# Optimization experiments

Measured on AMD Instinct MI355X. Metric: run time of the kernel, lower is better.

## Reference

```python
import jax, jax.numpy as jnp
import numpy as np

H = 3.0        # args.h smoothing length
N_NODES = 100000
DIM_HIDDEN = 128
D = 3


def setup_inputs() -> dict:
    key = jax.random.key(0)
    ks = jax.random.split(key, 10)
    E = 1600000
    v = jax.random.normal(ks[0], (N_NODES, D), dtype=jnp.float32)
    r_ij = jax.random.normal(ks[1], (E, D), dtype=jnp.float32)
    edge_index = jax.random.randint(ks[2], (2, E), 0, N_NODES, dtype=jnp.int64)
    # teacher MLP params: [1+D] -> dim_hidden -> dim_hidden -> 1
    def lin(k, fan_in, fan_out):
        bound = 1.0 / np.sqrt(fan_in)
        kw, kb = jax.random.split(k)
        W = jax.random.uniform(kw, (fan_out, fan_in), jnp.float32, -bound, bound)
        b = jax.random.uniform(kb, (fan_out,), jnp.float32, -bound, bound)
        return W, b
    W0, b0 = lin(ks[3], 1 + D, DIM_HIDDEN)
    W1, b1 = lin(ks[4], DIM_HIDDEN, DIM_HIDDEN)
    W2, b2 = lin(ks[5], DIM_HIDDEN, 1)
    return {"v": v, "r_ij": r_ij, "W0": W0, "b0": b0, "W1": W1, "b1": b1,
            "W2": W2, "b2": b2, "edge_index": edge_index}


def _teacher(x, W0, b0, W1, b1, W2, b2):
    x = jax.nn.silu(x @ W0.T + b0)
    x = jax.nn.silu(x @ W1.T + b1)
    return x @ W2.T + b2  # [E, 1]


def _scatter_mean(x, idx, n):
    s = jax.ops.segment_sum(x, idx, num_segments=n)
    c = jax.ops.segment_sum(jnp.ones((idx.shape[0], 1), x.dtype), idx, num_segments=n)
    return s / jnp.maximum(c, 1.0)


def reference(v, r_ij, W0, b0, W1, b1, W2, b2, edge_index):
    i = edge_index[0]
    j = edge_index[1]
    v_ij = v[i] - v[j]                                   # [E, D] gather-diff
    r_ = jnp.sqrt(jnp.sum(r_ij * r_ij, axis=-1, keepdims=True)) / H  # [E, 1]
    m_i = _teacher(jnp.concatenate([r_, v_ij], axis=-1), W0, b0, W1, b1, W2, b2)
    m_j = _teacher(jnp.concatenate([r_, -v_ij], axis=-1), W0, b0, W1, b1, W2, b2)
    S = _scatter_mean(m_i, i, N_NODES) + _scatter_mean(m_j, j, N_NODES)  # [N, 1]
    return S
```

## Files before the change

### kernel.cpp

```cpp
#include <hip/hip_runtime.h>

typedef unsigned short ushort_t;
typedef __bf16 bf16x8 __attribute__((ext_vector_type(8)));
typedef __bf16 bf16x2 __attribute__((ext_vector_type(2)));
typedef float f32x4 __attribute__((ext_vector_type(4)));

__device__ __forceinline__ ushort_t f2bf(float f) {
    unsigned u;
    __builtin_memcpy(&u, &f, 4);
    u += 0x7fffu + ((u >> 16) & 1u);
    return (ushort_t)(u >> 16);
}

__device__ __forceinline__ float silu(float x) {
    float e = __builtin_amdgcn_exp2f(x * -1.442695040888963f);
    return x * __builtin_amdgcn_rcpf(1.0f + e);
}

__device__ __forceinline__ float rdlane(float v, int l) {
    return __builtin_bit_cast(float, __builtin_amdgcn_readlane(__builtin_bit_cast(int, v), l));
}


#define CNT_UNIT 65536.0

__global__ __launch_bounds__(256, 2) void mlp_kernel(
    const float* __restrict__ v,
    const float* __restrict__ rij,
    const float* __restrict__ W0,
    const float* __restrict__ b0,
    const float* __restrict__ W1,
    const float* __restrict__ b1,
    const float* __restrict__ W2,
    const float* __restrict__ b2,
    const int* __restrict__ eidx,
    double* __restrict__ acc_i, double* __restrict__ acc_j,
    int E, int nchunks)
{
    __shared__ ushort_t sW1[16384];
    __shared__ ushort_t sH0[16384];

    const int tid  = threadIdx.x;
    const int lane = tid & 63;
    const int wave = tid >> 6;

    {
        int n = tid >> 1, half = tid & 1;
        const float* src = W1 + n * 128;
#pragma unroll
        for (int dk = 0; dk < 8; dk++) {
            int k0   = half * 64 + dk * 8;
            int frag = (n >> 4) * 4 + (k0 >> 5);
            int slot = (n & 15) + 16 * ((k0 >> 3) & 3);
            ushort_t tmp[8];
#pragma unroll
            for (int t = 0; t < 8; t++) tmp[t] = f2bf(src[k0 + t]);
            *(uint4*)(&sW1[frag * 512 + slot * 8]) = *(const uint4*)tmp;
        }
    }

    float4 w0q[2]; float b0v[2];
#pragma unroll
    for (int kk = 0; kk < 2; kk++) {
        int h = 2 * lane + kk;
        w0q[kk].x = W0[h * 4 + 0];
        w0q[kk].y = W0[h * 4 + 1];
        w0q[kk].z = W0[h * 4 + 2];
        w0q[kk].w = W0[h * 4 + 3];
        b0v[kk]   = b0[h];
    }
    float b1v[8], w2v[8];
#pragma unroll
    for (int nt = 0; nt < 8; nt++) {
        int ccol = nt * 16 + (lane & 15);
        b1v[nt] = b1[ccol];
        w2v[nt] = W2[ccol];
    }
    const float b2f = b2[0];

    __syncthreads();

    const int q = lane >> 4, c = lane & 15, p = (lane >> 2) & 3, bsub = lane & 3;
    const int ple  = lane >> 2;
    const int comp = lane & 3;

    auto preload = [&](int ch, float& val_o, int& idx_o) {
        float val = 0.f; int idxr = 0;
        int pe = ch * 64 + wave * 16 + ple;
        if (ch < nchunks && pe < E) {
            if (comp == 3) {
                float r0 = rij[3 * pe], r1 = rij[3 * pe + 1], r2 = rij[3 * pe + 2];
                val = sqrtf(fmaf(r0, r0, fmaf(r1, r1, r2 * r2))) * (1.0f / 3.0f);
            } else {
                int i = eidx[pe], jj = eidx[E + pe];
                idxr = (comp == 1) ? jj : i;
                val = v[3 * i + comp] - v[3 * jj + comp];
            }
        }
        val_o = val; idx_o = idxr;
    };

    float val; int idxr;
    preload(blockIdx.x, val, idxr);

    for (int chunk = blockIdx.x; chunk < nchunks; chunk += gridDim.x) {
        const float val_cur = val;
        const int   idx_cur = idxr;
        preload(chunk + (int)gridDim.x, val, idxr);

        const int ebase = chunk * 64 + wave * 16;

#pragma unroll
        for (int le = 0; le < 16; le++) {
            float vx = rdlane(val_cur, le * 4 + 0);
            float vy = rdlane(val_cur, le * 4 + 1);
            float vz = rdlane(val_cur, le * 4 + 2);
            float rr = rdlane(val_cur, le * 4 + 3);
            float si[2], sj[2];
#pragma unroll
            for (int kk = 0; kk < 2; kk++) {
                float cc = fmaf(w0q[kk].x, rr, b0v[kk]);
                float dd = fmaf(w0q[kk].y, vx, fmaf(w0q[kk].z, vy, w0q[kk].w * vz));
                si[kk] = silu(cc + dd);
                sj[kk] = silu(cc - dd);
            }
            bf16x2 pki, pkj;
            pki[0] = (__bf16)si[0]; pki[1] = (__bf16)si[1];
            pkj[0] = (__bf16)sj[0]; pkj[1] = (__bf16)sj[1];
            int mi = wave * 32 + 2 * le;
            int fr_i = ((mi >> 4) << 2) + q;
            int fr_j = (((mi + 1) >> 4) << 2) + q;
            int sl_i = (((mi & 15) ^ q ^ (p << 2)) & 15) + (p << 4);
            int sl_j = ((((mi + 1) & 15) ^ q ^ (p << 2)) & 15) + (p << 4);
            ((unsigned*)sH0)[fr_i * 256 + sl_i * 4 + bsub] = __builtin_bit_cast(unsigned, pki);
            ((unsigned*)sH0)[fr_j * 256 + sl_j * 4 + bsub] = __builtin_bit_cast(unsigned, pkj);
        }

        f32x4 acc[2][8];
#pragma unroll
        for (int t = 0; t < 2; t++)
#pragma unroll
            for (int nt = 0; nt < 8; nt++)
                acc[t][nt] = (f32x4){0.f, 0.f, 0.f, 0.f};

#pragma unroll
        for (int ks = 0; ks < 4; ks++) {
            int sl_rd = (((lane & 15) ^ ks ^ (q << 2)) & 15) + 16 * q;
            bf16x8 a0 = *(const bf16x8*)(&sH0[((2 * wave + 0) * 4 + ks) * 512 + sl_rd * 8]);
            bf16x8 a1 = *(const bf16x8*)(&sH0[((2 * wave + 1) * 4 + ks) * 512 + sl_rd * 8]);
#pragma unroll
            for (int nt = 0; nt < 8; nt++) {
                bf16x8 bb = *(const bf16x8*)(&sW1[(nt * 4 + ks) * 512 + lane * 8]);
                acc[0][nt] = __builtin_amdgcn_mfma_f32_16x16x32_bf16(a0, bb, acc[0][nt], 0, 0, 0);
                acc[1][nt] = __builtin_amdgcn_mfma_f32_16x16x32_bf16(a1, bb, acc[1][nt], 0, 0, 0);
            }
        }

        float rs[2][4] = {{0.f, 0.f, 0.f, 0.f}, {0.f, 0.f, 0.f, 0.f}};
#pragma unroll
        for (int t = 0; t < 2; t++)
#pragma unroll
            for (int nt = 0; nt < 8; nt++)
#pragma unroll
                for (int r = 0; r < 4; r++) {
                    float x = acc[t][nt][r] + b1v[nt];
                    rs[t][r] = fmaf(silu(x), w2v[nt], rs[t][r]);
                }
#pragma unroll
        for (int t = 0; t < 2; t++)
#pragma unroll
            for (int r = 0; r < 4; r++) {
                float s = rs[t][r];
                s += __shfl_xor(s, 1, 64);
                s += __shfl_xor(s, 2, 64);
                s += __shfl_xor(s, 4, 64);
                s += __shfl_xor(s, 8, 64);
                int el  = t * 8 + q * 2 + (r >> 1);
                int src = el * 4 + (r & 1);
                int node = __shfl(idx_cur, src, 64);
                int e = ebase + el;
                if (c == 0 && e < E) {
                    double contrib = (double)(s + b2f) + CNT_UNIT;
                    if (r & 1) atomicAdd(&acc_j[node], contrib);
                    else       atomicAdd(&acc_i[node], contrib);
                }
            }
    }
}

__global__ void finalize_kernel(const double* __restrict__ acc_i,
                                const double* __restrict__ acc_j,
                                float* __restrict__ out, int N)
{
    int n = blockIdx.x * 256 + threadIdx.x;
    if (n < N) {
        double ti = acc_i[n], tj = acc_j[n];
        double ci = rint(ti * (1.0 / CNT_UNIT));
        double cj = rint(tj * (1.0 / CNT_UNIT));
        double si = ti - ci * CNT_UNIT;
        double sj = tj - cj * CNT_UNIT;
        out[n] = (float)(si / fmax(ci, 1.0) + sj / fmax(cj, 1.0));
    }
}

extern "C" void kernel_launch(void* const* d_in, const int* in_sizes, int n_in,
                              void* d_out, int out_size, void* d_ws, size_t ws_size,
                              hipStream_t stream) {
    const float* v   = (const float*)d_in[0];
    const float* rij = (const float*)d_in[1];
    const float* W0  = (const float*)d_in[2];
    const float* b0  = (const float*)d_in[3];
    const float* W1  = (const float*)d_in[4];
    const float* b1  = (const float*)d_in[5];
    const float* W2  = (const float*)d_in[6];
    const float* b2  = (const float*)d_in[7];
    const int* eidx  = (const int*)d_in[8];

    const int E = in_sizes[1] / 3;
    const int N = out_size;

    double* acc_i = (double*)d_ws;
    double* acc_j = acc_i + N;

    hipMemsetAsync(d_ws, 0, (size_t)2 * N * sizeof(double), stream);

    int nchunks = (E + 63) / 64;
    int grid = nchunks < 512 ? nchunks : 512;
    mlp_kernel<<<grid, 256, 0, stream>>>(v, rij, W0, b0, W1, b1, W2, b2, eidx,
                                         acc_i, acc_j, E, nchunks);
    finalize_kernel<<<(N + 255) / 256, 256, 0, stream>>>(acc_i, acc_j,
                                                         (float*)d_out, N);
}
```

Before: 425.6 us.

## Fold log2e into weights, halve LDS staging, raise occupancy to three blocks

```diff
diff --git a/kernel.cpp b/kernel.cpp
--- a/kernel.cpp
+++ b/kernel.cpp
@@ -4,6 +4,9 @@
 typedef __bf16 bf16x8 __attribute__((ext_vector_type(8)));
 typedef __bf16 bf16x2 __attribute__((ext_vector_type(2)));
 typedef float f32x4 __attribute__((ext_vector_type(4)));
+
+#define LOG2E 1.4426950408889634f
+#define LN2   0.6931471805599453f
 
 __device__ __forceinline__ ushort_t f2bf(float f) {
     unsigned u;
@@ -12,9 +15,9 @@
     return (ushort_t)(u >> 16);
 }
 
-__device__ __forceinline__ float silu(float x) {
-    float e = __builtin_amdgcn_exp2f(x * -1.442695040888963f);
-    return x * __builtin_amdgcn_rcpf(1.0f + e);
+__device__ __forceinline__ float silu2(float y) {
+    float e = __builtin_amdgcn_exp2f(-y);
+    return y * __builtin_amdgcn_rcpf(1.0f + e);
 }
 
 __device__ __forceinline__ float rdlane(float v, int l) {
@@ -24,7 +27,7 @@
 
 #define CNT_UNIT 65536.0
 
-__global__ __launch_bounds__(256, 2) void mlp_kernel(
+__global__ __launch_bounds__(256, 3) void mlp_kernel(
     const float* __restrict__ v,
     const float* __restrict__ rij,
     const float* __restrict__ W0,
@@ -38,7 +41,7 @@
     int E, int nchunks)
 {
     __shared__ ushort_t sW1[16384];
-    __shared__ ushort_t sH0[16384];
+    __shared__ ushort_t sH0[8192];
 
     const int tid  = threadIdx.x;
     const int lane = tid & 63;
@@ -63,18 +66,18 @@
 #pragma unroll
     for (int kk = 0; kk < 2; kk++) {
         int h = 2 * lane + kk;
-        w0q[kk].x = W0[h * 4 + 0];
-        w0q[kk].y = W0[h * 4 + 1];
-        w0q[kk].z = W0[h * 4 + 2];
-        w0q[kk].w = W0[h * 4 + 3];
-        b0v[kk]   = b0[h];
+        w0q[kk].x = W0[h * 4 + 0] * LOG2E;
+        w0q[kk].y = W0[h * 4 + 1] * LOG2E;
+        w0q[kk].z = W0[h * 4 + 2] * LOG2E;
+        w0q[kk].w = W0[h * 4 + 3] * LOG2E;
+        b0v[kk]   = b0[h] * LOG2E;
     }
     float b1v[8], w2v[8];
 #pragma unroll
     for (int nt = 0; nt < 8; nt++) {
         int ccol = nt * 16 + (lane & 15);
-        b1v[nt] = b1[ccol];
-        w2v[nt] = W2[ccol];
+        b1v[nt] = b1[ccol] * LOG2E;
+        w2v[nt] = W2[ccol] * LN2;
     }
     const float b2f = b2[0];
 
@@ -110,30 +113,39 @@
 
         const int ebase = chunk * 64 + wave * 16;
 
-#pragma unroll
-        for (int le = 0; le < 16; le++) {
-            float vx = rdlane(val_cur, le * 4 + 0);
-            float vy = rdlane(val_cur, le * 4 + 1);
-            float vz = rdlane(val_cur, le * 4 + 2);
-            float rr = rdlane(val_cur, le * 4 + 3);
-            float si[2], sj[2];
-#pragma unroll
-            for (int kk = 0; kk < 2; kk++) {
-                float cc = fmaf(w0q[kk].x, rr, b0v[kk]);
-                float dd = fmaf(w0q[kk].y, vx, fmaf(w0q[kk].z, vy, w0q[kk].w * vz));
-                si[kk] = silu(cc + dd);
-                sj[kk] = silu(cc - dd);
-            }
-            bf16x2 pki, pkj;
-            pki[0] = (__bf16)si[0]; pki[1] = (__bf16)si[1];
-            pkj[0] = (__bf16)sj[0]; pkj[1] = (__bf16)sj[1];
-            int mi = wave * 32 + 2 * le;
-            int fr_i = ((mi >> 4) << 2) + q;
-            int fr_j = (((mi + 1) >> 4) << 2) + q;
-            int sl_i = (((mi & 15) ^ q ^ (p << 2)) & 15) + (p << 4);
-            int sl_j = ((((mi + 1) & 15) ^ q ^ (p << 2)) & 15) + (p << 4);
-            ((unsigned*)sH0)[fr_i * 256 + sl_i * 4 + bsub] = __builtin_bit_cast(unsigned, pki);
-            ((unsigned*)sH0)[fr_j * 256 + sl_j * 4 + bsub] = __builtin_bit_cast(unsigned, pkj);
+        bf16x8 afr[2][4];
+#pragma unroll
+        for (int half = 0; half < 2; ++half) {
+#pragma unroll
+            for (int le = 0; le < 8; le++) {
+                int se = half * 8 + le;
+                float vx = rdlane(val_cur, se * 4 + 0);
+                float vy = rdlane(val_cur, se * 4 + 1);
+                float vz = rdlane(val_cur, se * 4 + 2);
+                float rr = rdlane(val_cur, se * 4 + 3);
+                float si_[2], sj_[2];
+#pragma unroll
+                for (int kk = 0; kk < 2; kk++) {
+                    float cc = fmaf(w0q[kk].x, rr, b0v[kk]);
+                    float dd = fmaf(w0q[kk].y, vx, fmaf(w0q[kk].z, vy, w0q[kk].w * vz));
+                    si_[kk] = silu2(cc + dd);
+                    sj_[kk] = silu2(cc - dd);
+                }
+                bf16x2 pki, pkj;
+                pki[0] = (__bf16)si_[0]; pki[1] = (__bf16)si_[1];
+                pkj[0] = (__bf16)sj_[0]; pkj[1] = (__bf16)sj_[1];
+                int mi = 2 * le;
+                int fr = wave * 4 + q;
+                int sli = ((mi ^ q ^ (p << 2)) & 15) + (p << 4);
+                int slj = (((mi + 1) ^ q ^ (p << 2)) & 15) + (p << 4);
+                ((unsigned*)sH0)[fr * 256 + sli * 4 + bsub] = __builtin_bit_cast(unsigned, pki);
+                ((unsigned*)sH0)[fr * 256 + slj * 4 + bsub] = __builtin_bit_cast(unsigned, pkj);
+            }
+#pragma unroll
+            for (int ks = 0; ks < 4; ks++) {
+                int sl_rd = (((lane & 15) ^ ks ^ (q << 2)) & 15) + 16 * q;
+                afr[half][ks] = *(const bf16x8*)(&sH0[(wave * 4 + ks) * 512 + sl_rd * 8]);
+            }
         }
 
         f32x4 acc[2][8];
@@ -141,18 +153,15 @@
         for (int t = 0; t < 2; t++)
 #pragma unroll
             for (int nt = 0; nt < 8; nt++)
-                acc[t][nt] = (f32x4){0.f, 0.f, 0.f, 0.f};
+                acc[t][nt] = (f32x4){b1v[nt], b1v[nt], b1v[nt], b1v[nt]};
 
 #pragma unroll
         for (int ks = 0; ks < 4; ks++) {
-            int sl_rd = (((lane & 15) ^ ks ^ (q << 2)) & 15) + 16 * q;
-            bf16x8 a0 = *(const bf16x8*)(&sH0[((2 * wave + 0) * 4 + ks) * 512 + sl_rd * 8]);
-            bf16x8 a1 = *(const bf16x8*)(&sH0[((2 * wave + 1) * 4 + ks) * 512 + sl_rd * 8]);
 #pragma unroll
             for (int nt = 0; nt < 8; nt++) {
                 bf16x8 bb = *(const bf16x8*)(&sW1[(nt * 4 + ks) * 512 + lane * 8]);
-                acc[0][nt] = __builtin_amdgcn_mfma_f32_16x16x32_bf16(a0, bb, acc[0][nt], 0, 0, 0);
-                acc[1][nt] = __builtin_amdgcn_mfma_f32_16x16x32_bf16(a1, bb, acc[1][nt], 0, 0, 0);
+                acc[0][nt] = __builtin_amdgcn_mfma_f32_16x16x32_bf16(afr[0][ks], bb, acc[0][nt], 0, 0, 0);
+                acc[1][nt] = __builtin_amdgcn_mfma_f32_16x16x32_bf16(afr[1][ks], bb, acc[1][nt], 0, 0, 0);
             }
         }
 
@@ -163,8 +172,8 @@
             for (int nt = 0; nt < 8; nt++)
 #pragma unroll
                 for (int r = 0; r < 4; r++) {
-                    float x = acc[t][nt][r] + b1v[nt];
-                    rs[t][r] = fmaf(silu(x), w2v[nt], rs[t][r]);
+                    float x = acc[t][nt][r];
+                    rs[t][r] = fmaf(silu2(x), w2v[nt], rs[t][r]);
                 }
 #pragma unroll
         for (int t = 0; t < 2; t++)
@@ -225,7 +234,7 @@
     hipMemsetAsync(d_ws, 0, (size_t)2 * N * sizeof(double), stream);
 
     int nchunks = (E + 63) / 64;
-    int grid = nchunks < 512 ? nchunks : 512;
+    int grid = nchunks < 768 ? nchunks : 768;
     mlp_kernel<<<grid, 256, 0, stream>>>(v, rij, W0, b0, W1, b1, W2, b2, eidx,
                                          acc_i, acc_j, E, nchunks);
     finalize_kernel<<<(N + 255) / 256, 256, 0, stream>>>(acc_i, acc_j,
```

New measurement: 381.1 us. -10.5%, faster.
